# Kernel tuning notes

Measured on AMD Instinct MI355X. Metric: run time of the kernel, lower is better.

The kernel has to match this reference:

```python
import jax, jax.numpy as jnp
import numpy as np

ATT_DIM = 512
HEADS = 8
HEAD_DIM = ATT_DIM // HEADS
D_IN = 512
LEFT_MASK = 256
RIGHT_MASK = 0
LARGE = 1e30


def pos_encoding(S, d):
    # Transformer-XL sinusoid table over relative positions S-1 .. -(S-1), length 2S-1.
    inv_freq = (1.0 / (10000.0 ** (np.arange(0, d, 2.0) / d))).astype(np.float32)
    pos = jnp.arange(S - 1, -S, -1, dtype=jnp.float32)          # [2S-1]
    ang = pos[:, None] * jnp.asarray(inv_freq)[None, :]          # [2S-1, d/2]
    # concat([sin, cos], -1) on a trailing singleton -> interleaved sin/cos per frequency
    return jnp.stack([jnp.sin(ang), jnp.cos(ang)], axis=-1).reshape(2 * S - 1, d)


def rel_shift(x):
    # x: [B, N, S, 2S-1] -> [B, N, S, S] with out[i, j] = x[i, S-1 - i + j]
    B, N, S, L = x.shape
    x = jnp.pad(x, ((0, 0), (0, 0), (0, 0), (1, 0)))             # [B,N,S,L+1]
    x = x.reshape(B, N, L + 1, S)[:, :, 1:, :]                   # [B,N,L,S]
    x = x.reshape(B, N, S, L)
    return x[:, :, :, :S]


def setup_inputs() -> dict:
    key = jax.random.key(0)
    ks = jax.random.split(key, 9)
    B, S, D = 2, 2048, D_IN
    scale = 0.02
    return {
        "x": jax.random.normal(ks[0], (B, S, D), dtype=jnp.float32),
        "Wq": jax.random.normal(ks[1], (D, ATT_DIM), dtype=jnp.float32) * scale,
        "b_con": jax.random.normal(ks[2], (ATT_DIM,), dtype=jnp.float32) * scale,
        "b_rel": jax.random.normal(ks[3], (ATT_DIM,), dtype=jnp.float32) * scale,
        "Wk": jax.random.normal(ks[4], (D, ATT_DIM), dtype=jnp.float32) * scale,
        "Wkr": jax.random.normal(ks[5], (D_IN, ATT_DIM), dtype=jnp.float32) * scale,
        "Wv": jax.random.normal(ks[6], (D, ATT_DIM), dtype=jnp.float32) * scale,
        "bv": jax.random.normal(ks[7], (ATT_DIM,), dtype=jnp.float32) * scale,
        "x_len": jax.random.randint(ks[8], (B,), 1, S + 1).astype(jnp.int32),
    }


def reference(x, Wq, b_con, b_rel, Wk, Wkr, Wv, bv, x_len):
    B, S, D = x.shape
    N, Dh = HEADS, HEAD_DIM

    # content/relative query share the kernel (TiedDense) with separate biases
    q_lin = jnp.einsum('bsd,de->bse', x, Wq)
    q_con = (q_lin + b_con).reshape(B, S, N, Dh)
    q_rel = (q_lin + b_rel).reshape(B, S, N, Dh)
    k_con = jnp.einsum('bsd,de->bse', x, Wk).reshape(B, S, N, Dh)

    content_energy = jnp.einsum('bind,bjnd->bnij', q_con, k_con)  # [B,N,S,S]

    pos_emb = pos_encoding(S, D_IN)                               # [2S-1, D]
    k_rel = (pos_emb @ Wkr).reshape(2 * S - 1, N, Dh)
    relative_energy = jnp.einsum('bind,jnd->bnij', q_rel, k_rel)  # [B,N,S,2S-1]
    relative_energy = rel_shift(relative_energy)                  # [B,N,S,S]

    energy = (content_energy + relative_energy) / jnp.sqrt(jnp.float32(Dh))

    # sequence mask over keys (broadcast [B,1,1,S]) * banded mask (band_part)
    j = jnp.arange(S)
    seq_mask = (j[None, :] < x_len[:, None]).astype(jnp.float32)[:, None, None, :]
    i = jnp.arange(S)[:, None]
    band = ((i - j[None, :] <= LEFT_MASK) & (j[None, :] - i <= RIGHT_MASK)).astype(jnp.float32)
    mask = seq_mask * band[None, None, :, :]

    masked_energy = energy - (1.0 - mask) * LARGE
    attention = jax.nn.softmax(masked_energy, axis=-1)

    v = (jnp.einsum('bsd,de->bse', x, Wv) + bv).reshape(B, S, N, Dh)
    context = jnp.einsum('bnij,bjnd->bind', attention, v).reshape(B, S, N * Dh)
    return context
```

## Files before the change

kernel.cpp:

```cpp
#include <hip/hip_runtime.h>
#include <math.h>

#define S_ 2048
#define NH 8
#define DH 64
#define RSTRIDE 264
#define LP 72

typedef __attribute__((ext_vector_type(8))) short short8;
typedef __attribute__((ext_vector_type(4))) float f32x4;
typedef unsigned short ushort_t;

__device__ __forceinline__ short bf16r(float x) {
    union { float f; unsigned u; } v; v.f = x;
    unsigned r = v.u + 0x7fffu + ((v.u >> 16) & 1u);
    return (short)(r >> 16);
}
__device__ __forceinline__ float b2f(ushort_t h) {
    union { float f; unsigned u; } v; v.u = ((unsigned)h) << 16; return v.f;
}

__global__ __launch_bounds__(256) void wtrans_kernel(
    const float* __restrict__ Wq, const float* __restrict__ Wk,
    const float* __restrict__ Wv, const float* __restrict__ Wkr,
    ushort_t* __restrict__ WTq, ushort_t* __restrict__ WTk,
    ushort_t* __restrict__ WTv, ushort_t* __restrict__ WTkr)
{
    const int widx = blockIdx.z;
    const float* W = (widx == 0) ? Wq : (widx == 1) ? Wk : (widx == 2) ? Wv : Wkr;
    ushort_t* WT   = (widx == 0) ? WTq : (widx == 1) ? WTk : (widx == 2) ? WTv : WTkr;
    const int k0 = blockIdx.x * 64, n0 = blockIdx.y * 64;
    __shared__ __align__(16) ushort_t T[64][72];
    const int t = threadIdx.x;
    const int srow = t >> 2, sc0 = (t & 3) * 16;
    const float* src = &W[(size_t)(k0 + srow) * 512 + n0 + sc0];
#pragma unroll
    for (int u = 0; u < 16; ++u) T[sc0 + u][srow] = (ushort_t)bf16r(src[u]);
    __syncthreads();
    ushort_t* dst = &WT[(size_t)(n0 + srow) * 512 + k0 + sc0];
    *(short8*)dst       = *(const short8*)&T[srow][sc0];
    *(short8*)(dst + 8) = *(const short8*)&T[srow][sc0 + 8];
}

__global__ __launch_bounds__(256) void pos_kernel(ushort_t* __restrict__ pos)
{
    const int r = blockIdx.x, f = threadIdx.x;
    const float C = -0.051905126482615036f;
    unsigned pk = 0;
    if (r <= 256) {
        float ang = (float)r * exp2f(C * (float)f);
        unsigned s = (unsigned)(ushort_t)bf16r(sinf(ang));
        unsigned c = (unsigned)(ushort_t)bf16r(cosf(ang));
        pk = s | (c << 16);
    }
    ((unsigned*)pos)[(size_t)r * 256 + f] = pk;
}

__global__ __launch_bounds__(256) void qkv_gemm(
    const float* __restrict__ x,
    const ushort_t* __restrict__ WTq, const ushort_t* __restrict__ WTk,
    const ushort_t* __restrict__ WTv,
    const float* __restrict__ b_con, const float* __restrict__ b_rel,
    const float* __restrict__ bv,
    ushort_t* __restrict__ qcon, ushort_t* __restrict__ qrel,
    ushort_t* __restrict__ kout, ushort_t* __restrict__ vout)
{
    const int m0 = blockIdx.x * 128;
    const int widx = blockIdx.y >> 3;
    const int n0 = (blockIdx.y & 7) * 64;
    const ushort_t* WT = (widx == 0) ? WTq : (widx == 1) ? WTk : WTv;
    const int tid = threadIdx.x, lane = tid & 63, w = tid >> 6;
    const int quad = lane >> 4, l16 = lane & 15;

    __shared__ __align__(16) ushort_t A_lds[128][40];
    __shared__ __align__(16) ushort_t B_lds[64][40];

    f32x4 acc[2][4];
#pragma unroll
    for (int mt = 0; mt < 2; ++mt)
#pragma unroll
        for (int nt = 0; nt < 4; ++nt) acc[mt][nt] = (f32x4){0.f, 0.f, 0.f, 0.f};

    const int arow = tid >> 1, ak0 = (tid & 1) * 16;
    const int brow = tid >> 2, bk0 = (tid & 3) * 8;

    for (int k0 = 0; k0 < 512; k0 += 32) {
        const float* xs = &x[(size_t)(m0 + arow) * 512 + k0 + ak0];
        ushort_t t16[16];
#pragma unroll
        for (int u = 0; u < 16; ++u) t16[u] = (ushort_t)bf16r(xs[u]);
        *(short8*)&A_lds[arow][ak0]     = *(short8*)&t16[0];
        *(short8*)&A_lds[arow][ak0 + 8] = *(short8*)&t16[8];
        *(short8*)&B_lds[brow][bk0] =
            *(const short8*)&WT[(size_t)(n0 + brow) * 512 + k0 + bk0];
        __syncthreads();

        short8 a0 = *(const short8*)&A_lds[w * 32 + l16][quad * 8];
        short8 a1 = *(const short8*)&A_lds[w * 32 + 16 + l16][quad * 8];
#pragma unroll
        for (int nt = 0; nt < 4; ++nt) {
            short8 bb = *(const short8*)&B_lds[nt * 16 + l16][quad * 8];
            acc[0][nt] = __builtin_amdgcn_mfma_f32_16x16x32_bf16(a0, bb, acc[0][nt], 0, 0, 0);
            acc[1][nt] = __builtin_amdgcn_mfma_f32_16x16x32_bf16(a1, bb, acc[1][nt], 0, 0, 0);
        }
        __syncthreads();
    }

#pragma unroll
    for (int nt = 0; nt < 4; ++nt) {
        const int col = n0 + nt * 16 + l16;
        float bc = 0.f, br = 0.f;
        if (widx == 0) { bc = b_con[col]; br = b_rel[col]; }
        else if (widx == 2) { bc = bv[col]; }
#pragma unroll
        for (int mt = 0; mt < 2; ++mt) {
#pragma unroll
            for (int reg = 0; reg < 4; ++reg) {
                const size_t m = (size_t)(m0 + w * 32 + mt * 16 + quad * 4 + reg);
                const float val = acc[mt][nt][reg];
                if (widx == 0) {
                    qcon[m * 512 + col] = (ushort_t)bf16r((val + bc) * 0.125f);
                    qrel[m * 512 + col] = (ushort_t)bf16r((val + br) * 0.125f);
                } else if (widx == 1) {
                    kout[m * 512 + col] = (ushort_t)bf16r(val);
                } else {
                    vout[m * 512 + col] = (ushort_t)bf16r(val + bc);
                }
            }
        }
    }
}

__global__ __launch_bounds__(256) void krel_gemm(
    const ushort_t* __restrict__ pos, const ushort_t* __restrict__ WTkr,
    ushort_t* __restrict__ krel)
{
    const int m0 = blockIdx.x * 128;
    const int n0 = blockIdx.y * 64;
    const int tid = threadIdx.x, lane = tid & 63, w = tid >> 6;
    const int quad = lane >> 4, l16 = lane & 15;

    __shared__ __align__(16) ushort_t A_lds[128][40];
    __shared__ __align__(16) ushort_t B_lds[64][40];

    f32x4 acc[2][4];
#pragma unroll
    for (int mt = 0; mt < 2; ++mt)
#pragma unroll
        for (int nt = 0; nt < 4; ++nt) acc[mt][nt] = (f32x4){0.f, 0.f, 0.f, 0.f};

    const int arow = tid >> 1, ak0 = (tid & 1) * 16;
    const int brow = tid >> 2, bk0 = (tid & 3) * 8;

    for (int k0 = 0; k0 < 512; k0 += 32) {
        const ushort_t* ps = &pos[(size_t)(m0 + arow) * 512 + k0 + ak0];
        *(short8*)&A_lds[arow][ak0]     = *(const short8*)ps;
        *(short8*)&A_lds[arow][ak0 + 8] = *(const short8*)(ps + 8);
        *(short8*)&B_lds[brow][bk0] =
            *(const short8*)&WTkr[(size_t)(n0 + brow) * 512 + k0 + bk0];
        __syncthreads();

        short8 a0 = *(const short8*)&A_lds[w * 32 + l16][quad * 8];
        short8 a1 = *(const short8*)&A_lds[w * 32 + 16 + l16][quad * 8];
#pragma unroll
        for (int nt = 0; nt < 4; ++nt) {
            short8 bb = *(const short8*)&B_lds[nt * 16 + l16][quad * 8];
            acc[0][nt] = __builtin_amdgcn_mfma_f32_16x16x32_bf16(a0, bb, acc[0][nt], 0, 0, 0);
            acc[1][nt] = __builtin_amdgcn_mfma_f32_16x16x32_bf16(a1, bb, acc[1][nt], 0, 0, 0);
        }
        __syncthreads();
    }

#pragma unroll
    for (int nt = 0; nt < 4; ++nt) {
        const int col = n0 + nt * 16 + l16;
#pragma unroll
        for (int mt = 0; mt < 2; ++mt)
#pragma unroll
            for (int reg = 0; reg < 4; ++reg) {
                const size_t m = (size_t)(m0 + w * 32 + mt * 16 + quad * 4 + reg);
                krel[m * 512 + col] = (ushort_t)bf16r(acc[mt][nt][reg]);
            }
    }
}

__global__ __launch_bounds__(256) void rel_gemm(
    const ushort_t* __restrict__ qrel, const ushort_t* __restrict__ krel,
    float* __restrict__ R)
{
    const int tile = blockIdx.x, n = blockIdx.y, b = blockIdx.z;
    const int i0 = tile * 128;
    const int tid = threadIdx.x, lane = tid & 63, w = tid >> 6;
    const int quad = lane >> 4, l16 = lane & 15;

    __shared__ __align__(16) ushort_t A_lds[128][LP];
    __shared__ __align__(16) ushort_t B_lds[64][LP];

    {
        const int srow = tid >> 1, sc0 = (tid & 1) * 32;
        const ushort_t* src = &qrel[((size_t)b * S_ + i0 + srow) * 512 + n * 64 + sc0];
#pragma unroll
        for (int u = 0; u < 4; ++u)
            *(short8*)&A_lds[srow][sc0 + u * 8] = *(const short8*)(src + u * 8);
    }

    const size_t rbase = ((size_t)(b * NH + n) * S_ + i0) * RSTRIDE;
    const int srow2 = tid >> 2, sc2 = (tid & 3) * 16;

#pragma unroll 1
    for (int rc = 0; rc < 5; ++rc) {
        __syncthreads();
        {
            const ushort_t* src = &krel[(size_t)(rc * 64 + srow2) * 512 + n * 64 + sc2];
            *(short8*)&B_lds[srow2][sc2]     = *(const short8*)src;
            *(short8*)&B_lds[srow2][sc2 + 8] = *(const short8*)(src + 8);
        }
        __syncthreads();

        short8 a[2][2];
#pragma unroll
        for (int mt = 0; mt < 2; ++mt) {
            a[mt][0] = *(const short8*)&A_lds[w * 32 + mt * 16 + l16][quad * 8];
            a[mt][1] = *(const short8*)&A_lds[w * 32 + mt * 16 + l16][quad * 8 + 32];
        }
#pragma unroll
        for (int nt = 0; nt < 4; ++nt) {
            short8 b0 = *(const short8*)&B_lds[nt * 16 + l16][quad * 8];
            short8 b1 = *(const short8*)&B_lds[nt * 16 + l16][quad * 8 + 32];
            const int r = rc * 64 + nt * 16 + l16;
#pragma unroll
            for (int mt = 0; mt < 2; ++mt) {
                f32x4 s = (f32x4){0.f, 0.f, 0.f, 0.f};
                s = __builtin_amdgcn_mfma_f32_16x16x32_bf16(a[mt][0], b0, s, 0, 0, 0);
                s = __builtin_amdgcn_mfma_f32_16x16x32_bf16(a[mt][1], b1, s, 0, 0, 0);
                if (r < RSTRIDE) {
#pragma unroll
                    for (int reg = 0; reg < 4; ++reg) {
                        const int i = w * 32 + mt * 16 + quad * 4 + reg;
                        R[rbase + (size_t)i * RSTRIDE + r] = s[reg];
                    }
                }
            }
        }
    }
}

__global__ __launch_bounds__(512) void vmean_kernel(
    const ushort_t* __restrict__ v, float* __restrict__ vmean)
{
    const int b = blockIdx.x, sc = blockIdx.y;
    const int e = threadIdx.x;
    float sum = 0.f;
    for (int s = sc * 64; s < sc * 64 + 64; ++s)
        sum += b2f(v[((size_t)b * S_ + s) * 512 + e]);
    atomicAdd(&vmean[(size_t)b * 512 + e], sum * (1.0f / (float)S_));
}

__global__ __launch_bounds__(256) void attn_kernel(
    const ushort_t* __restrict__ qcon, const ushort_t* __restrict__ kbuf,
    const ushort_t* __restrict__ vbuf, const float* __restrict__ R,
    const float* __restrict__ vmean, const int* __restrict__ xlen_p,
    float* __restrict__ out)
{
    const int tile = blockIdx.x, n = blockIdx.y, b = blockIdx.z;
    const int i0 = tile * 64;
    const int tid = threadIdx.x, lane = tid & 63, w = tid >> 6;
    const int quad = lane >> 4, l16 = lane & 15;
    const int xlen = xlen_p[b];

    __shared__ __align__(16) ushort_t q_lds[64][LP];
    __shared__ __align__(16) ushort_t k_lds[64][LP];
    __shared__ __align__(16) ushort_t vT_lds[64][LP];
    __shared__ __align__(16) ushort_t p_lds[64][LP];

    const int srow = tid >> 2, sc0 = (tid & 3) * 16;

    {
        const ushort_t* src = &qcon[((size_t)b * S_ + i0 + srow) * 512 + n * 64 + sc0];
        *(short8*)&q_lds[srow][sc0]     = *(const short8*)src;
        *(short8*)&q_lds[srow][sc0 + 8] = *(const short8*)(src + 8);
    }

    f32x4 Oa[4];
#pragma unroll
    for (int nt = 0; nt < 4; ++nt) Oa[nt] = (f32x4){0.f, 0.f, 0.f, 0.f};
    float lpart[4] = {};

    const size_t rrowB = (size_t)(b * NH + n) * S_ * RSTRIDE;

#pragma unroll 1
    for (int c = 0; c < 5; ++c) {
        const int jc0 = i0 - 256 + c * 64;
        __syncthreads();

        float rv[4][4];
#pragma unroll
        for (int jt = 0; jt < 4; ++jt) {
#pragma unroll
            for (int reg = 0; reg < 4; ++reg) {
                const int i = i0 + w * 16 + quad * 4 + reg;
                const int j = jc0 + jt * 16 + l16;
                const int r = i - j;
                const bool valid = (j >= 0) && (j < xlen) && (r >= 0) && (r <= 256);
                rv[jt][reg] = valid ? R[rrowB + (size_t)i * RSTRIDE + r] : 0.f;
            }
        }

        {
            const int jg = jc0 + srow;
            const bool ok = (jg >= 0);
            const ushort_t* ks = &kbuf[((size_t)b * S_ + jg) * 512 + n * 64 + sc0];
            const ushort_t* vs = &vbuf[((size_t)b * S_ + jg) * 512 + n * 64 + sc0];
            short8 z8 = {0, 0, 0, 0, 0, 0, 0, 0};
            *(short8*)&k_lds[srow][sc0]     = ok ? *(const short8*)ks : z8;
            *(short8*)&k_lds[srow][sc0 + 8] = ok ? *(const short8*)(ks + 8) : z8;
            ushort_t tv[16];
            *(short8*)&tv[0] = ok ? *(const short8*)vs : z8;
            *(short8*)&tv[8] = ok ? *(const short8*)(vs + 8) : z8;
#pragma unroll
            for (int u = 0; u < 16; ++u) vT_lds[sc0 + u][srow] = tv[u];
        }
        __syncthreads();

        short8 aq0 = *(const short8*)&q_lds[w * 16 + l16][quad * 8];
        short8 aq1 = *(const short8*)&q_lds[w * 16 + l16][quad * 8 + 32];
        f32x4 Sacc[4];
#pragma unroll
        for (int jt = 0; jt < 4; ++jt) {
            short8 bk0 = *(const short8*)&k_lds[jt * 16 + l16][quad * 8];
            short8 bk1 = *(const short8*)&k_lds[jt * 16 + l16][quad * 8 + 32];
            f32x4 s = (f32x4){0.f, 0.f, 0.f, 0.f};
            s = __builtin_amdgcn_mfma_f32_16x16x32_bf16(aq0, bk0, s, 0, 0, 0);
            s = __builtin_amdgcn_mfma_f32_16x16x32_bf16(aq1, bk1, s, 0, 0, 0);
            Sacc[jt] = s;
        }

#pragma unroll
        for (int jt = 0; jt < 4; ++jt) {
#pragma unroll
            for (int reg = 0; reg < 4; ++reg) {
                const int i = i0 + w * 16 + quad * 4 + reg;
                const int j = jc0 + jt * 16 + l16;
                const int r = i - j;
                const bool valid = (j >= 0) && (j < xlen) && (r >= 0) && (r <= 256);
                float e = valid ? __expf(Sacc[jt][reg] + rv[jt][reg]) : 0.f;
                lpart[reg] += e;
                p_lds[w * 16 + quad * 4 + reg][jt * 16 + l16] = (ushort_t)bf16r(e);
            }
        }
        __syncthreads();

        short8 ap0 = *(const short8*)&p_lds[w * 16 + l16][quad * 8];
        short8 ap1 = *(const short8*)&p_lds[w * 16 + l16][quad * 8 + 32];
#pragma unroll
        for (int nt = 0; nt < 4; ++nt) {
            short8 bv0 = *(const short8*)&vT_lds[nt * 16 + l16][quad * 8];
            short8 bv1 = *(const short8*)&vT_lds[nt * 16 + l16][quad * 8 + 32];
            Oa[nt] = __builtin_amdgcn_mfma_f32_16x16x32_bf16(ap0, bv0, Oa[nt], 0, 0, 0);
            Oa[nt] = __builtin_amdgcn_mfma_f32_16x16x32_bf16(ap1, bv1, Oa[nt], 0, 0, 0);
        }
    }

#pragma unroll
    for (int reg = 0; reg < 4; ++reg) {
#pragma unroll
        for (int off = 1; off < 16; off <<= 1)
            lpart[reg] += __shfl_xor(lpart[reg], off, 64);
    }

#pragma unroll
    for (int reg = 0; reg < 4; ++reg) {
        const int i = i0 + w * 16 + quad * 4 + reg;
        const bool dead = (i >= xlen + 256);
        const float linv = 1.0f / lpart[reg];
#pragma unroll
        for (int nt = 0; nt < 4; ++nt) {
            const int d = n * 64 + nt * 16 + l16;
            float val = dead ? vmean[(size_t)b * 512 + d] : Oa[nt][reg] * linv;
            out[((size_t)b * S_ + i) * 512 + d] = val;
        }
    }
}

extern "C" void kernel_launch(void* const* d_in, const int* in_sizes, int n_in,
                              void* d_out, int out_size, void* d_ws, size_t ws_size,
                              hipStream_t stream) {
    const float* x     = (const float*)d_in[0];
    const float* Wq    = (const float*)d_in[1];
    const float* b_con = (const float*)d_in[2];
    const float* b_rel = (const float*)d_in[3];
    const float* Wk    = (const float*)d_in[4];
    const float* Wkr   = (const float*)d_in[5];
    const float* Wv    = (const float*)d_in[6];
    const float* bv    = (const float*)d_in[7];
    const int*   xlen  = (const int*)d_in[8];
    float* out = (float*)d_out;

    float* ws = (float*)d_ws;
    float* vmean = ws;
    float* R     = vmean + 1024;
    ushort_t* ub   = (ushort_t*)(R + 8650752);
    ushort_t* qcon = ub;
    ushort_t* kbuf = qcon + 2097152;
    ushort_t* vbuf = kbuf + 2097152;
    ushort_t* qrel = vbuf + 2097152;
    ushort_t* krel = qrel + 2097152;
    ushort_t* pos  = krel + 196608;
    ushort_t* WTq  = pos  + 196608;
    ushort_t* WTk  = WTq + 262144;
    ushort_t* WTv  = WTk + 262144;
    ushort_t* WTkr = WTv + 262144;

    hipMemsetAsync(vmean, 0, 1024 * sizeof(float), stream);

    wtrans_kernel<<<dim3(8, 8, 4), 256, 0, stream>>>(Wq, Wk, Wv, Wkr,
                                                     WTq, WTk, WTv, WTkr);
    pos_kernel<<<384, 256, 0, stream>>>(pos);
    qkv_gemm<<<dim3(32, 24), 256, 0, stream>>>(x, WTq, WTk, WTv, b_con, b_rel, bv,
                                               qcon, qrel, kbuf, vbuf);
    krel_gemm<<<dim3(3, 8), 256, 0, stream>>>(pos, WTkr, krel);
    rel_gemm<<<dim3(16, 8, 2), 256, 0, stream>>>(qrel, krel, R);
    vmean_kernel<<<dim3(2, 32), 512, 0, stream>>>(vbuf, vmean);
    attn_kernel<<<dim3(32, 8, 2), 256, 0, stream>>>(qcon, kbuf, vbuf, R, vmean,
                                                    xlen, out);
}
```

Before: 150.5 us.

## Store V transposed, R in bf16, merge prep kernels, shrink attention tiles

The V projection is now written in a per-head transposed layout, so the attention kernel loads V^T tiles with vector loads instead of scattering a transpose through LDS, and vmean becomes a simple row reduction with no atomics and no memset. The relative-energy buffer R is stored as bf16 instead of fp32, halving its write and read traffic. The weight transpose and positional table kernels are merged into one launch. The attention kernel uses 32-row query tiles with 128 threads, doubling the block count for better occupancy. The risks are extra bf16 rounding on the relative energies and strided 8-byte scattered stores for V^T in the QKV GEMM.

```diff
diff --git a/kernel.cpp b/kernel.cpp
--- a/kernel.cpp
+++ b/kernel.cpp
@@ -8,6 +8,7 @@
 #define LP 72
 
 typedef __attribute__((ext_vector_type(8))) short short8;
+typedef __attribute__((ext_vector_type(4))) short short4v;
 typedef __attribute__((ext_vector_type(4))) float f32x4;
 typedef unsigned short ushort_t;
 
@@ -20,18 +21,37 @@
     union { float f; unsigned u; } v; v.u = ((unsigned)h) << 16; return v.f;
 }
 
-__global__ __launch_bounds__(256) void wtrans_kernel(
+__global__ __launch_bounds__(256) void prep_kernel(
     const float* __restrict__ Wq, const float* __restrict__ Wk,
     const float* __restrict__ Wv, const float* __restrict__ Wkr,
     ushort_t* __restrict__ WTq, ushort_t* __restrict__ WTk,
-    ushort_t* __restrict__ WTv, ushort_t* __restrict__ WTkr)
+    ushort_t* __restrict__ WTv, ushort_t* __restrict__ WTkr,
+    ushort_t* __restrict__ pos)
 {
     const int widx = blockIdx.z;
+    const int t = threadIdx.x;
+    if (widx == 4) {
+        const int base = blockIdx.y * 8 + blockIdx.x;
+        const float C = -0.051905126482615036f;
+        const int f = t;
+#pragma unroll
+        for (int rep = 0; rep < 6; ++rep) {
+            const int r = base + rep * 64;
+            unsigned pk = 0;
+            if (r <= 256) {
+                float ang = (float)r * exp2f(C * (float)f);
+                unsigned s = (unsigned)(ushort_t)bf16r(sinf(ang));
+                unsigned c = (unsigned)(ushort_t)bf16r(cosf(ang));
+                pk = s | (c << 16);
+            }
+            ((unsigned*)pos)[(size_t)r * 256 + f] = pk;
+        }
+        return;
+    }
     const float* W = (widx == 0) ? Wq : (widx == 1) ? Wk : (widx == 2) ? Wv : Wkr;
     ushort_t* WT   = (widx == 0) ? WTq : (widx == 1) ? WTk : (widx == 2) ? WTv : WTkr;
     const int k0 = blockIdx.x * 64, n0 = blockIdx.y * 64;
     __shared__ __align__(16) ushort_t T[64][72];
-    const int t = threadIdx.x;
     const int srow = t >> 2, sc0 = (t & 3) * 16;
     const float* src = &W[(size_t)(k0 + srow) * 512 + n0 + sc0];
 #pragma unroll
@@ -40,20 +60,6 @@
     ushort_t* dst = &WT[(size_t)(n0 + srow) * 512 + k0 + sc0];
     *(short8*)dst       = *(const short8*)&T[srow][sc0];
     *(short8*)(dst + 8) = *(const short8*)&T[srow][sc0 + 8];
-}
-
-__global__ __launch_bounds__(256) void pos_kernel(ushort_t* __restrict__ pos)
-{
-    const int r = blockIdx.x, f = threadIdx.x;
-    const float C = -0.051905126482615036f;
-    unsigned pk = 0;
-    if (r <= 256) {
-        float ang = (float)r * exp2f(C * (float)f);
-        unsigned s = (unsigned)(ushort_t)bf16r(sinf(ang));
-        unsigned c = (unsigned)(ushort_t)bf16r(cosf(ang));
-        pk = s | (c << 16);
-    }
-    ((unsigned*)pos)[(size_t)r * 256 + f] = pk;
 }
 
 __global__ __launch_bounds__(256) void qkv_gemm(
@@ -63,7 +69,7 @@
     const float* __restrict__ b_con, const float* __restrict__ b_rel,
     const float* __restrict__ bv,
     ushort_t* __restrict__ qcon, ushort_t* __restrict__ qrel,
-    ushort_t* __restrict__ kout, ushort_t* __restrict__ vout)
+    ushort_t* __restrict__ kout, ushort_t* __restrict__ vT)
 {
     const int m0 = blockIdx.x * 128;
     const int widx = blockIdx.y >> 3;
@@ -114,17 +120,26 @@
         else if (widx == 2) { bc = bv[col]; }
 #pragma unroll
         for (int mt = 0; mt < 2; ++mt) {
-#pragma unroll
-            for (int reg = 0; reg < 4; ++reg) {
-                const size_t m = (size_t)(m0 + w * 32 + mt * 16 + quad * 4 + reg);
-                const float val = acc[mt][nt][reg];
-                if (widx == 0) {
-                    qcon[m * 512 + col] = (ushort_t)bf16r((val + bc) * 0.125f);
-                    qrel[m * 512 + col] = (ushort_t)bf16r((val + br) * 0.125f);
-                } else if (widx == 1) {
-                    kout[m * 512 + col] = (ushort_t)bf16r(val);
-                } else {
-                    vout[m * 512 + col] = (ushort_t)bf16r(val + bc);
+            if (widx == 2) {
+                const int j0 = m0 + w * 32 + mt * 16 + quad * 4;
+                const int b = j0 >> 11, s0 = j0 & 2047;
+                const int n = col >> 6, d = col & 63;
+                short4v h;
+#pragma unroll
+                for (int reg = 0; reg < 4; ++reg)
+                    h[reg] = bf16r(acc[mt][nt][reg] + bc);
+                *(short4v*)&vT[((size_t)((b * NH + n) * 64 + d)) * 2048 + s0] = h;
+            } else {
+#pragma unroll
+                for (int reg = 0; reg < 4; ++reg) {
+                    const size_t m = (size_t)(m0 + w * 32 + mt * 16 + quad * 4 + reg);
+                    const float val = acc[mt][nt][reg];
+                    if (widx == 0) {
+                        qcon[m * 512 + col] = (ushort_t)bf16r((val + bc) * 0.125f);
+                        qrel[m * 512 + col] = (ushort_t)bf16r((val + br) * 0.125f);
+                    } else {
+                        kout[m * 512 + col] = (ushort_t)bf16r(val);
+                    }
                 }
             }
         }
@@ -186,7 +201,7 @@
 
 __global__ __launch_bounds__(256) void rel_gemm(
     const ushort_t* __restrict__ qrel, const ushort_t* __restrict__ krel,
-    float* __restrict__ R)
+    ushort_t* __restrict__ R)
 {
     const int tile = blockIdx.x, n = blockIdx.y, b = blockIdx.z;
     const int i0 = tile * 128;
@@ -237,7 +252,7 @@
 #pragma unroll
                     for (int reg = 0; reg < 4; ++reg) {
                         const int i = w * 32 + mt * 16 + quad * 4 + reg;
-                        R[rbase + (size_t)i * RSTRIDE + r] = s[reg];
+                        R[rbase + (size_t)i * RSTRIDE + r] = (ushort_t)bf16r(s[reg]);
                     }
                 }
             }
@@ -245,40 +260,47 @@
     }
 }
 
-__global__ __launch_bounds__(512) void vmean_kernel(
-    const ushort_t* __restrict__ v, float* __restrict__ vmean)
-{
-    const int b = blockIdx.x, sc = blockIdx.y;
-    const int e = threadIdx.x;
+__global__ __launch_bounds__(256) void vmean_kernel(
+    const ushort_t* __restrict__ vT, float* __restrict__ vmean)
+{
+    const int row = blockIdx.x * 4 + (threadIdx.x >> 6);
+    const int lane = threadIdx.x & 63;
+    const ushort_t* src = &vT[(size_t)row * 2048 + lane * 8];
     float sum = 0.f;
-    for (int s = sc * 64; s < sc * 64 + 64; ++s)
-        sum += b2f(v[((size_t)b * S_ + s) * 512 + e]);
-    atomicAdd(&vmean[(size_t)b * 512 + e], sum * (1.0f / (float)S_));
-}
-
-__global__ __launch_bounds__(256) void attn_kernel(
+#pragma unroll
+    for (int it = 0; it < 4; ++it) {
+        short8 h = *(const short8*)(src + it * 512);
+#pragma unroll
+        for (int u = 0; u < 8; ++u) sum += b2f((ushort_t)h[u]);
+    }
+#pragma unroll
+    for (int off = 32; off >= 1; off >>= 1)
+        sum += __shfl_xor(sum, off, 64);
+    if (lane == 0) vmean[row] = sum * (1.0f / (float)S_);
+}
+
+__global__ __launch_bounds__(128) void attn_kernel(
     const ushort_t* __restrict__ qcon, const ushort_t* __restrict__ kbuf,
-    const ushort_t* __restrict__ vbuf, const float* __restrict__ R,
+    const ushort_t* __restrict__ vT, const ushort_t* __restrict__ R,
     const float* __restrict__ vmean, const int* __restrict__ xlen_p,
     float* __restrict__ out)
 {
     const int tile = blockIdx.x, n = blockIdx.y, b = blockIdx.z;
-    const int i0 = tile * 64;
+    const int i0 = tile * 32;
     const int tid = threadIdx.x, lane = tid & 63, w = tid >> 6;
     const int quad = lane >> 4, l16 = lane & 15;
     const int xlen = xlen_p[b];
 
-    __shared__ __align__(16) ushort_t q_lds[64][LP];
+    __shared__ __align__(16) ushort_t q_lds[32][LP];
     __shared__ __align__(16) ushort_t k_lds[64][LP];
     __shared__ __align__(16) ushort_t vT_lds[64][LP];
-    __shared__ __align__(16) ushort_t p_lds[64][LP];
-
-    const int srow = tid >> 2, sc0 = (tid & 3) * 16;
+    __shared__ __align__(16) ushort_t p_lds[32][LP];
 
     {
-        const ushort_t* src = &qcon[((size_t)b * S_ + i0 + srow) * 512 + n * 64 + sc0];
-        *(short8*)&q_lds[srow][sc0]     = *(const short8*)src;
-        *(short8*)&q_lds[srow][sc0 + 8] = *(const short8*)(src + 8);
+        const int qr = tid >> 2, qc = (tid & 3) * 16;
+        const ushort_t* src = &qcon[((size_t)b * S_ + i0 + qr) * 512 + n * 64 + qc];
+        *(short8*)&q_lds[qr][qc]     = *(const short8*)src;
+        *(short8*)&q_lds[qr][qc + 8] = *(const short8*)(src + 8);
     }
 
     f32x4 Oa[4];
@@ -287,6 +309,9 @@
     float lpart[4] = {};
 
     const size_t rrowB = (size_t)(b * NH + n) * S_ * RSTRIDE;
+    const size_t vTbase = (size_t)((b * NH + n) * 64) * 2048;
+
+    const int srow = tid >> 1, sc0 = (tid & 1) * 32;
 
 #pragma unroll 1
     for (int c = 0; c < 5; ++c) {
@@ -302,23 +327,24 @@
                 const int j = jc0 + jt * 16 + l16;
                 const int r = i - j;
                 const bool valid = (j >= 0) && (j < xlen) && (r >= 0) && (r <= 256);
-                rv[jt][reg] = valid ? R[rrowB + (size_t)i * RSTRIDE + r] : 0.f;
+                rv[jt][reg] = valid ? b2f(R[rrowB + (size_t)i * RSTRIDE + r]) : 0.f;
             }
         }
 
         {
             const int jg = jc0 + srow;
-            const bool ok = (jg >= 0);
+            const bool okk = (jg >= 0);
             const ushort_t* ks = &kbuf[((size_t)b * S_ + jg) * 512 + n * 64 + sc0];
-            const ushort_t* vs = &vbuf[((size_t)b * S_ + jg) * 512 + n * 64 + sc0];
+            const ushort_t* vs = &vT[vTbase + (size_t)srow * 2048 + jc0 + sc0];
             short8 z8 = {0, 0, 0, 0, 0, 0, 0, 0};
-            *(short8*)&k_lds[srow][sc0]     = ok ? *(const short8*)ks : z8;
-            *(short8*)&k_lds[srow][sc0 + 8] = ok ? *(const short8*)(ks + 8) : z8;
-            ushort_t tv[16];
-            *(short8*)&tv[0] = ok ? *(const short8*)vs : z8;
-            *(short8*)&tv[8] = ok ? *(const short8*)(vs + 8) : z8;
-#pragma unroll
-            for (int u = 0; u < 16; ++u) vT_lds[sc0 + u][srow] = tv[u];
+#pragma unroll
+            for (int u = 0; u < 4; ++u) {
+                *(short8*)&k_lds[srow][sc0 + u * 8] =
+                    okk ? *(const short8*)(ks + u * 8) : z8;
+                const bool okv = (jc0 + sc0 + u * 8) >= 0;
+                *(short8*)&vT_lds[srow][sc0 + u * 8] =
+                    okv ? *(const short8*)(vs + u * 8) : z8;
+            }
         }
         __syncthreads();
 
@@ -398,12 +424,12 @@
 
     float* ws = (float*)d_ws;
     float* vmean = ws;
-    float* R     = vmean + 1024;
-    ushort_t* ub   = (ushort_t*)(R + 8650752);
-    ushort_t* qcon = ub;
+    ushort_t* ub   = (ushort_t*)(vmean + 1024);
+    ushort_t* R    = ub;
+    ushort_t* qcon = R    + 8650752;
     ushort_t* kbuf = qcon + 2097152;
-    ushort_t* vbuf = kbuf + 2097152;
-    ushort_t* qrel = vbuf + 2097152;
+    ushort_t* vT   = kbuf + 2097152;
+    ushort_t* qrel = vT   + 2097152;
     ushort_t* krel = qrel + 2097152;
     ushort_t* pos  = krel + 196608;
     ushort_t* WTq  = pos  + 196608;
@@ -411,16 +437,13 @@
     ushort_t* WTv  = WTk + 262144;
     ushort_t* WTkr = WTv + 262144;
 
-    hipMemsetAsync(vmean, 0, 1024 * sizeof(float), stream);
-
-    wtrans_kernel<<<dim3(8, 8, 4), 256, 0, stream>>>(Wq, Wk, Wv, Wkr,
-                                                     WTq, WTk, WTv, WTkr);
-    pos_kernel<<<384, 256, 0, stream>>>(pos);
+    prep_kernel<<<dim3(8, 8, 5), 256, 0, stream>>>(Wq, Wk, Wv, Wkr,
+                                                   WTq, WTk, WTv, WTkr, pos);
     qkv_gemm<<<dim3(32, 24), 256, 0, stream>>>(x, WTq, WTk, WTv, b_con, b_rel, bv,
-                                               qcon, qrel, kbuf, vbuf);
+                                               qcon, qrel, kbuf, vT);
     krel_gemm<<<dim3(3, 8), 256, 0, stream>>>(pos, WTkr, krel);
     rel_gemm<<<dim3(16, 8, 2), 256, 0, stream>>>(qrel, krel, R);
-    vmean_kernel<<<dim3(2, 32), 512, 0, stream>>>(vbuf, vmean);
-    attn_kernel<<<dim3(32, 8, 2), 256, 0, stream>>>(qcon, kbuf, vbuf, R, vmean,
+    vmean_kernel<<<256, 256, 0, stream>>>(vT, vmean);
+    attn_kernel<<<dim3(64, 8, 2), 128, 0, stream>>>(qcon, kbuf, vT, R, vmean,
                                                     xlen, out);
 }
```

Result: slower. 165.5 us (+10.0%).
